# Kernel optimization log

Measured on AMD Instinct MI355X. Metric: run time of the kernel, lower is better.

## Reference

```python
import jax, jax.numpy as jnp
import numpy as np

N = 200000   # active voxels
B = 2        # batch size
G = 128      # spatial grid extent per axis
CIN = 64
COUT = 64
KS = 3       # kernel size -> 27 offsets
DIL = 1
EPS = 1e-5


def setup_inputs() -> dict:
    rng = np.random.default_rng(0)
    # unique active voxel coordinates over a B x G^3 grid
    lin = rng.choice(B * G * G * G, size=N, replace=False)
    b = lin // (G * G * G)
    r = lin % (G * G * G)
    x = r // (G * G)
    r2 = r % (G * G)
    y = r2 // G
    z = r2 % G
    coords = jnp.asarray(np.stack([b, x, y, z], axis=1).astype(np.int32))
    key = jax.random.key(0)
    ks = jax.random.split(key, 7)
    feats = jax.random.normal(ks[0], (N, CIN), jnp.float32)
    s1 = 1.0 / np.sqrt(KS ** 3 * CIN)
    s2 = 1.0 / np.sqrt(KS ** 3 * COUT)
    return {
        "feats": feats,
        "w1": jax.random.normal(ks[1], (KS ** 3, CIN, COUT), jnp.float32) * s1,
        "g1": 1.0 + 0.1 * jax.random.normal(ks[2], (COUT,), jnp.float32),
        "b1": 0.1 * jax.random.normal(ks[3], (COUT,), jnp.float32),
        "w2": jax.random.normal(ks[4], (KS ** 3, COUT, COUT), jnp.float32) * s2,
        "g2": 1.0 + 0.1 * jax.random.normal(ks[5], (COUT,), jnp.float32),
        "b2": 0.1 * jax.random.normal(ks[6], (COUT,), jnp.float32),
        "coords": coords,
    }


def build_neighbors(coords):
    """Hash (dense) lookup: for each of 27 kernel offsets, the input index of
    the neighboring active voxel (submanifold: output sites == input sites).
    Returns idx [27, N] int32 (0 where invalid) and mask [27, N] bool."""
    n = coords.shape[0]
    lin = ((coords[:, 0] * G + coords[:, 1]) * G + coords[:, 2]) * G + coords[:, 3]
    table = jnp.full((B * G * G * G,), -1, jnp.int32).at[lin].set(
        jnp.arange(n, dtype=jnp.int32))
    offs = jnp.asarray(
        [[dx, dy, dz] for dx in (-1, 0, 1) for dy in (-1, 0, 1) for dz in (-1, 0, 1)],
        dtype=jnp.int32) * DIL                       # [27, 3]
    nxyz = coords[None, :, 1:] + offs[:, None, :]    # [27, N, 3]
    inb = jnp.all((nxyz >= 0) & (nxyz < G), axis=-1)  # [27, N]
    c = jnp.clip(nxyz, 0, G - 1)
    nlin = ((coords[None, :, 0] * G + c[..., 0]) * G + c[..., 1]) * G + c[..., 2]
    idx = table[nlin]                                # [27, N]
    mask = inb & (idx >= 0)
    return jnp.where(mask, idx, 0), mask


def subm_conv(feats, nbr_idx, nbr_mask, w):
    # gather-GEMM-scatter, accumulated per kernel offset
    out = jnp.zeros((feats.shape[0], w.shape[-1]), feats.dtype)
    for k in range(w.shape[0]):
        g = jnp.where(nbr_mask[k][:, None], feats[nbr_idx[k]], 0.0)  # [N, Cin]
        out = out + g @ w[k]
    return out


def sparse_bn(x, gamma, beta):
    m = jnp.mean(x, axis=0)
    v = jnp.var(x, axis=0)
    return (x - m) * jax.lax.rsqrt(v + EPS) * gamma + beta


def reference(feats, w1, g1, b1, w2, g2, b2, coords):
    nbr_idx, nbr_mask = build_neighbors(coords)
    h = jax.nn.relu(sparse_bn(subm_conv(feats, nbr_idx, nbr_mask, w1), g1, b1))
    h = sparse_bn(subm_conv(h, nbr_idx, nbr_mask, w2), g2, b2)
    # shortcut is Identity (in_channels == out_channels, stride == 1)
    return jax.nn.relu(h + feats)
```

## Files before the change

kernel.cpp:

```cpp
#include <hip/hip_runtime.h>


constexpr int N_VOX = 200000;
constexpr int GEXT  = 128;
constexpr int C     = 64;
constexpr int K27   = 27;
constexpr int TBL_N = 2 * GEXT * GEXT * GEXT;
constexpr float EPSF = 1e-5f;

constexpr int NTILE = N_VOX / 16;
constexpr int NBLK  = 512;
constexpr int WHALF = K27 * 2 * 2 * 4 * 16 * 8;

using short8  = __attribute__((ext_vector_type(8))) short;
using floatx4 = __attribute__((ext_vector_type(4))) float;

static __device__ __forceinline__ ushort f2bf(float f) {
  union { float f; unsigned u; } a; a.f = f;
  unsigned r = a.u + 0x7fff + ((a.u >> 16) & 1);
  return (ushort)(r >> 16);
}
static __device__ __forceinline__ float bf2f(ushort h) {
  union { unsigned u; float f; } a; a.u = ((unsigned)h) << 16;
  return a.f;
}

__global__ __launch_bounds__(256) void k_fill_table(int* __restrict__ t,
                                                    ushort* __restrict__ zrow) {
  int i = blockIdx.x * 256 + threadIdx.x;
  if (i < TBL_N) t[i] = -1;
  if (i < 64) zrow[i] = 0;
}

__global__ __launch_bounds__(256) void k_scatter(const int* __restrict__ coords,
                                                 int* __restrict__ t) {
  int n = blockIdx.x * 256 + threadIdx.x;
  if (n >= N_VOX) return;
  int4 c = reinterpret_cast<const int4*>(coords)[n];
  int lin = ((c.x * GEXT + c.y) * GEXT + c.z) * GEXT + c.w;
  t[lin] = n;
}

__global__ __launch_bounds__(256) void k_nbr(const int* __restrict__ coords,
                                             const int* __restrict__ t,
                                             int* __restrict__ nbr) {
  int n = blockIdx.x * 256 + threadIdx.x;
  if (n >= N_VOX) return;
  int4 c = reinterpret_cast<const int4*>(coords)[n];
  int k = 0;
  #pragma unroll
  for (int dx = -1; dx <= 1; ++dx)
    #pragma unroll
    for (int dy = -1; dy <= 1; ++dy)
      #pragma unroll
      for (int dz = -1; dz <= 1; ++dz) {
        int x = c.y + dx, y = c.z + dy, z = c.w + dz;
        int idx = -1;
        if (((unsigned)x < (unsigned)GEXT) & ((unsigned)y < (unsigned)GEXT) &
            ((unsigned)z < (unsigned)GEXT)) {
          int lin = ((c.x * GEXT + x) * GEXT + y) * GEXT + z;
          idx = t[lin];
        }
        nbr[k * N_VOX + n] = idx;
        ++k;
      }
}

__global__ __launch_bounds__(256) void k_cast4(const float* __restrict__ in,
                                               ushort* __restrict__ out, int n4) {
  int i = blockIdx.x * 256 + threadIdx.x;
  if (i >= n4) return;
  float4 v = reinterpret_cast<const float4*>(in)[i];
  ushort4 o;
  o.x = f2bf(v.x); o.y = f2bf(v.y); o.z = f2bf(v.z); o.w = f2bf(v.w);
  reinterpret_cast<ushort4*>(out)[i] = o;
}

__global__ __launch_bounds__(256) void k_castw_p(const float* __restrict__ w,
                                                 ushort* __restrict__ wtp) {
  int i = blockIdx.x * 256 + threadIdx.x;
  if (i >= K27 * 4096) return;
  int k = i >> 12, r = i & 4095, ci = r >> 6, co = r & 63;
  int half = co >> 5, q = (co >> 4) & 1, row = co & 15;
  int ks = ci >> 5, cig = (ci >> 3) & 3, e = ci & 7;
  int dst = ((((half * K27 + k) * 2 + q) * 2 + ks) * 4 + cig) * 128 + row * 8 + e;
  wtp[dst] = f2bf(w[i]);
}

template <bool OUT_BF16>
__global__ __launch_bounds__(512, 1) void k_conv_sp(
    const ushort* __restrict__ fin,
    const ushort* __restrict__ wtp,
    const int* __restrict__ nbr,
    const ushort* __restrict__ zrow,
    void* __restrict__ fout,
    float* __restrict__ part) {
  __shared__ ushort Wl[WHALF];
  __shared__ float sred[8][4][16];

  const int tid  = threadIdx.x;
  const int lane = tid & 63;
  const int wv   = tid >> 6;
  const int half = blockIdx.x & 1;
  const int chunk = blockIdx.x >> 1;
  const int lo = lane & 15, hi = lane >> 4;

  {
    const uint4* src = (const uint4*)(wtp + (size_t)half * WHALF);
    uint4* dst = (uint4*)Wl;
    for (int i = tid; i < WHALF / 8; i += 512) dst[i] = src[i];
  }
  __syncthreads();

  const char* wbase = (const char*)Wl + lane * 16;
  float s8[8], ss8[8];
  #pragma unroll
  for (int j = 0; j < 8; ++j) { s8[j] = 0.f; ss8[j] = 0.f; }

  for (int t = chunk * 8 + wv; t < NTILE; t += 2048) {
    const int n0 = t * 16;
    floatx4 acc0 = {0.f, 0.f, 0.f, 0.f};
    floatx4 acc1 = {0.f, 0.f, 0.f, 0.f};

    int idxs[27];
    #pragma unroll
    for (int k = 0; k < K27; ++k) idxs[k] = nbr[k * N_VOX + n0 + lo];

    #pragma unroll
    for (int k = 0; k < K27; ++k) {
      int idx = idxs[k];
      if (__ballot(idx >= 0)) {
        const char* base = (idx >= 0)
            ? (const char*)fin + ((size_t)idx << 7)
            : (const char*)zrow;
        short8 b0 = *(const short8*)(base + hi * 16);
        short8 b1 = *(const short8*)(base + 64 + hi * 16);
        const char* wb = wbase + k * 4096;
        short8 a00 = *(const short8*)(wb);
        short8 a01 = *(const short8*)(wb + 1024);
        short8 a10 = *(const short8*)(wb + 2048);
        short8 a11 = *(const short8*)(wb + 3072);
        acc0 = __builtin_amdgcn_mfma_f32_16x16x32_bf16(a00, b0, acc0, 0, 0, 0);
        acc0 = __builtin_amdgcn_mfma_f32_16x16x32_bf16(a01, b1, acc0, 0, 0, 0);
        acc1 = __builtin_amdgcn_mfma_f32_16x16x32_bf16(a10, b0, acc1, 0, 0, 0);
        acc1 = __builtin_amdgcn_mfma_f32_16x16x32_bf16(a11, b1, acc1, 0, 0, 0);
      }
    }

    const int vox = n0 + lo;
    const int cb  = half * 32 + hi * 4;
    if (OUT_BF16) {
      ushort* o = (ushort*)fout + ((size_t)vox << 6) + cb;
      ushort4 v0, v1;
      v0.x = f2bf(acc0[0]); v0.y = f2bf(acc0[1]);
      v0.z = f2bf(acc0[2]); v0.w = f2bf(acc0[3]);
      v1.x = f2bf(acc1[0]); v1.y = f2bf(acc1[1]);
      v1.z = f2bf(acc1[2]); v1.w = f2bf(acc1[3]);
      *(ushort4*)o = v0;
      *(ushort4*)(o + 16) = v1;
    } else {
      float* o = (float*)fout + ((size_t)vox << 6) + cb;
      float4 v0 = {acc0[0], acc0[1], acc0[2], acc0[3]};
      float4 v1 = {acc1[0], acc1[1], acc1[2], acc1[3]};
      *(float4*)o = v0;
      *(float4*)(o + 16) = v1;
    }
    #pragma unroll
    for (int r = 0; r < 4; ++r) {
      s8[r]     += acc0[r];  ss8[r]     += acc0[r] * acc0[r];
      s8[4 + r] += acc1[r];  ss8[4 + r] += acc1[r] * acc1[r];
    }
  }

  #pragma unroll
  for (int j = 0; j < 8; ++j) {
    float s = s8[j], ss = ss8[j];
    #pragma unroll
    for (int m = 1; m < 16; m <<= 1) {
      s  += __shfl_xor(s, m);
      ss += __shfl_xor(ss, m);
    }
    if (lo == 0) { sred[wv][hi][j] = s; sred[wv][hi][8 + j] = ss; }
  }
  __syncthreads();
  if (tid < 64) {
    int h2 = tid >> 4, j = tid & 15;
    float v = 0.f;
    #pragma unroll
    for (int w = 0; w < 8; ++w) v += sred[w][h2][j];
    int j2 = j & 7;
    int c_local = ((j2 >> 2) << 4) + h2 * 4 + (j2 & 3);
    part[(size_t)blockIdx.x * 64 + (j < 8 ? c_local : 32 + c_local)] = v;
  }
}

__global__ __launch_bounds__(256) void k_bnfin(const float* __restrict__ part,
                                               const float* __restrict__ gamma,
                                               const float* __restrict__ beta,
                                               float* __restrict__ ab) {
  __shared__ float red[256][2];
  int tid = threadIdx.x;
  int c = tid & 63, g = tid >> 6;
  int half = c >> 5, lc = c & 31;
  float s = 0.f, ss = 0.f;
  for (int ch = g; ch < NBLK / 2; ch += 4) {
    const float* p = part + (size_t)(ch * 2 + half) * 64;
    s += p[lc]; ss += p[32 + lc];
  }
  red[tid][0] = s; red[tid][1] = ss;
  __syncthreads();
  if (tid < 64) {
    s  = red[tid][0] + red[tid + 64][0] + red[tid + 128][0] + red[tid + 192][0];
    ss = red[tid][1] + red[tid + 64][1] + red[tid + 128][1] + red[tid + 192][1];
    float mean = s / (float)N_VOX;
    float var  = ss / (float)N_VOX - mean * mean;
    float a = gamma[tid] * rsqrtf(var + EPSF);
    ab[tid]      = a;
    ab[64 + tid] = beta[tid] - mean * a;
  }
}

__global__ __launch_bounds__(256) void k_bnrelu_bf(ushort* __restrict__ x,
                                                   const float* __restrict__ ab) {
  int i = blockIdx.x * 256 + threadIdx.x;
  ushort4 v = reinterpret_cast<ushort4*>(x)[i];
  int cb = (i * 4) & 63;
  v.x = f2bf(fmaxf(bf2f(v.x) * ab[cb]     + ab[64 + cb],     0.f));
  v.y = f2bf(fmaxf(bf2f(v.y) * ab[cb + 1] + ab[64 + cb + 1], 0.f));
  v.z = f2bf(fmaxf(bf2f(v.z) * ab[cb + 2] + ab[64 + cb + 2], 0.f));
  v.w = f2bf(fmaxf(bf2f(v.w) * ab[cb + 3] + ab[64 + cb + 3], 0.f));
  reinterpret_cast<ushort4*>(x)[i] = v;
}

__global__ __launch_bounds__(256) void k_final4(float* __restrict__ h2,
                                                const ushort* __restrict__ fb,
                                                const float* __restrict__ ab) {
  int i = blockIdx.x * 256 + threadIdx.x;
  float4 a = reinterpret_cast<float4*>(h2)[i];
  ushort4 f = reinterpret_cast<const ushort4*>(fb)[i];
  int cb = (i * 4) & 63;
  float4 o;
  o.x = fmaxf(a.x * ab[cb]     + ab[64 + cb]     + bf2f(f.x), 0.f);
  o.y = fmaxf(a.y * ab[cb + 1] + ab[64 + cb + 1] + bf2f(f.y), 0.f);
  o.z = fmaxf(a.z * ab[cb + 2] + ab[64 + cb + 2] + bf2f(f.z), 0.f);
  o.w = fmaxf(a.w * ab[cb + 3] + ab[64 + cb + 3] + bf2f(f.w), 0.f);
  reinterpret_cast<float4*>(h2)[i] = o;
}

extern "C" void kernel_launch(void* const* d_in, const int* in_sizes, int n_in,
                              void* d_out, int out_size, void* d_ws, size_t ws_size,
                              hipStream_t stream) {
  const float* feats  = (const float*)d_in[0];
  const float* w1     = (const float*)d_in[1];
  const float* g1     = (const float*)d_in[2];
  const float* b1     = (const float*)d_in[3];
  const float* w2     = (const float*)d_in[4];
  const float* g2     = (const float*)d_in[5];
  const float* b2     = (const float*)d_in[6];
  const int*   coords = (const int*)d_in[7];
  float* out = (float*)d_out;

  char* ws = (char*)d_ws;
  int*    table = (int*)ws;     ws += (size_t)TBL_N * 4;
  int*    nbr   = (int*)ws;     ws += (size_t)K27 * N_VOX * 4;
  ushort* fb    = (ushort*)ws;  ws += (size_t)N_VOX * C * 2;
  ushort* h1    = (ushort*)ws;  ws += (size_t)N_VOX * C * 2;
  ushort* wtp1  = (ushort*)ws;  ws += (size_t)2 * WHALF * 2;
  ushort* wtp2  = (ushort*)ws;  ws += (size_t)2 * WHALF * 2;
  float*  part  = (float*)ws;   ws += (size_t)NBLK * 64 * 4;
  float*  ab1   = (float*)ws;   ws += 512;
  float*  ab2   = (float*)ws;   ws += 512;
  ushort* zrow  = (ushort*)ws;  ws += 128;

  const int NC4 = N_VOX * C / 4;
  const int VBLK = NC4 / 256;

  k_fill_table<<<(TBL_N + 255) / 256, 256, 0, stream>>>(table, zrow);
  k_scatter<<<(N_VOX + 255) / 256, 256, 0, stream>>>(coords, table);
  k_nbr<<<(N_VOX + 255) / 256, 256, 0, stream>>>(coords, table, nbr);

  k_cast4<<<VBLK, 256, 0, stream>>>(feats, fb, NC4);
  k_castw_p<<<(K27 * 4096 + 255) / 256, 256, 0, stream>>>(w1, wtp1);
  k_castw_p<<<(K27 * 4096 + 255) / 256, 256, 0, stream>>>(w2, wtp2);

  k_conv_sp<true><<<NBLK, 512, 0, stream>>>(fb, wtp1, nbr, zrow, h1, part);
  k_bnfin<<<1, 256, 0, stream>>>(part, g1, b1, ab1);
  k_bnrelu_bf<<<VBLK, 256, 0, stream>>>(h1, ab1);

  k_conv_sp<false><<<NBLK, 512, 0, stream>>>(h1, wtp2, nbr, zrow, out, part);
  k_bnfin<<<1, 256, 0, stream>>>(part, g2, b2, ab2);
  k_final4<<<VBLK, 256, 0, stream>>>(out, fb, ab2);
}
```

Measured before the change: 343.5 us.

## Reorder voxels spatially, switch conv to 32x32 MFMA with global weights

Builds a spatially sorted permutation of voxels (count, scan, compact over the hash table) and runs both convolutions in that order, so neighbour gathers hit nearby rows and the cache works better. The conv kernel now uses 32x32x16 bf16 MFMA reading weights straight from global memory instead of staging them in LDS. It launches one block per 128 voxels with an XCD-aware block mapping and higher occupancy, and scatters the final output back through the permutation. The residual now reads fp32 feats directly. This adds several preprocessing kernels and relies on the weight reads being served from cache.

```diff
diff --git a/kernel.cpp b/kernel.cpp
--- a/kernel.cpp
+++ b/kernel.cpp
@@ -7,13 +7,10 @@
 constexpr int K27   = 27;
 constexpr int TBL_N = 2 * GEXT * GEXT * GEXT;
 constexpr float EPSF = 1e-5f;
-
-constexpr int NTILE = N_VOX / 16;
-constexpr int NBLK  = 512;
-constexpr int WHALF = K27 * 2 * 2 * 4 * 16 * 8;
-
-using short8  = __attribute__((ext_vector_type(8))) short;
-using floatx4 = __attribute__((ext_vector_type(4))) float;
+constexpr int NCBLK = 1563;
+
+using short8   = __attribute__((ext_vector_type(8))) short;
+using floatx16 = __attribute__((ext_vector_type(16))) float;
 
 static __device__ __forceinline__ ushort f2bf(float f) {
   union { float f; unsigned u; } a; a.f = f;
@@ -25,10 +22,12 @@
   return a.f;
 }
 
-__global__ __launch_bounds__(256) void k_fill_table(int* __restrict__ t,
-                                                    ushort* __restrict__ zrow) {
+__global__ __launch_bounds__(256) void k_fill(int* __restrict__ t,
+                                              int* __restrict__ bsum,
+                                              ushort* __restrict__ zrow) {
   int i = blockIdx.x * 256 + threadIdx.x;
   if (i < TBL_N) t[i] = -1;
+  if (i < 4096) bsum[i] = 0;
   if (i < 64) zrow[i] = 0;
 }
 
@@ -41,12 +40,66 @@
   t[lin] = n;
 }
 
-__global__ __launch_bounds__(256) void k_nbr(const int* __restrict__ coords,
-                                             const int* __restrict__ t,
-                                             int* __restrict__ nbr) {
+__global__ __launch_bounds__(256) void k_count(const int* __restrict__ coords,
+                                               int* __restrict__ bsum) {
   int n = blockIdx.x * 256 + threadIdx.x;
   if (n >= N_VOX) return;
   int4 c = reinterpret_cast<const int4*>(coords)[n];
+  int lin = ((c.x * GEXT + c.y) * GEXT + c.z) * GEXT + c.w;
+  atomicAdd(&bsum[lin >> 10], 1);
+}
+
+__global__ __launch_bounds__(1024) void k_scan(const int* __restrict__ bsum,
+                                               int* __restrict__ boff) {
+  __shared__ int sc[1024];
+  int t = threadIdx.x;
+  int v0 = bsum[t * 4], v1 = bsum[t * 4 + 1], v2 = bsum[t * 4 + 2],
+      v3 = bsum[t * 4 + 3];
+  int s = v0 + v1 + v2 + v3;
+  sc[t] = s;
+  __syncthreads();
+  for (int off = 1; off < 1024; off <<= 1) {
+    int x = (t >= off) ? sc[t - off] : 0;
+    __syncthreads();
+    sc[t] += x;
+    __syncthreads();
+  }
+  int excl = sc[t] - s;
+  boff[t * 4]     = excl;
+  boff[t * 4 + 1] = excl + v0;
+  boff[t * 4 + 2] = excl + v0 + v1;
+  boff[t * 4 + 3] = excl + v0 + v1 + v2;
+}
+
+__global__ __launch_bounds__(1024) void k_compact(int* __restrict__ table,
+                                                  const int* __restrict__ boff,
+                                                  int* __restrict__ perm) {
+  __shared__ int wsum[16];
+  int i = blockIdx.x * 1024 + threadIdx.x;
+  int orig = table[i];
+  bool valid = orig >= 0;
+  unsigned long long bal = __ballot(valid);
+  int lane = threadIdx.x & 63, wv = threadIdx.x >> 6;
+  int before = __popcll(bal & ((1ull << lane) - 1ull));
+  if (lane == 0) wsum[wv] = __popcll(bal);
+  __syncthreads();
+  int woff = 0;
+  for (int w = 0; w < 16; ++w) woff += (w < wv) ? wsum[w] : 0;
+  if (valid) {
+    int j = boff[blockIdx.x] + woff + before;
+    perm[j] = orig;
+    table[i] = j;
+  }
+}
+
+__global__ __launch_bounds__(256) void k_nbrp(const int* __restrict__ coords,
+                                              const int* __restrict__ table,
+                                              const int* __restrict__ perm,
+                                              int* __restrict__ nbrp) {
+  int j = blockIdx.x * 256 + threadIdx.x;
+  if (j >= N_VOX) return;
+  int orig = perm[j];
+  int4 c = reinterpret_cast<const int4*>(coords)[orig];
   int k = 0;
   #pragma unroll
   for (int dx = -1; dx <= 1; ++dx)
@@ -55,142 +108,129 @@
       #pragma unroll
       for (int dz = -1; dz <= 1; ++dz) {
         int x = c.y + dx, y = c.z + dy, z = c.w + dz;
-        int idx = -1;
+        int rank = -1;
         if (((unsigned)x < (unsigned)GEXT) & ((unsigned)y < (unsigned)GEXT) &
             ((unsigned)z < (unsigned)GEXT)) {
           int lin = ((c.x * GEXT + x) * GEXT + y) * GEXT + z;
-          idx = t[lin];
+          rank = table[lin];
         }
-        nbr[k * N_VOX + n] = idx;
+        nbrp[k * N_VOX + j] = rank;
         ++k;
       }
 }
 
-__global__ __launch_bounds__(256) void k_cast4(const float* __restrict__ in,
-                                               ushort* __restrict__ out, int n4) {
-  int i = blockIdx.x * 256 + threadIdx.x;
-  if (i >= n4) return;
-  float4 v = reinterpret_cast<const float4*>(in)[i];
+__global__ __launch_bounds__(256) void k_gcast(const float* __restrict__ feats,
+                                               const int* __restrict__ perm,
+                                               ushort* __restrict__ fbp) {
+  int i = blockIdx.x * 256 + threadIdx.x;
+  int j = i >> 4, seg = i & 15;
+  int p = perm[j];
+  float4 v = reinterpret_cast<const float4*>(feats)[(p << 4) + seg];
   ushort4 o;
   o.x = f2bf(v.x); o.y = f2bf(v.y); o.z = f2bf(v.z); o.w = f2bf(v.w);
-  reinterpret_cast<ushort4*>(out)[i] = o;
-}
-
-__global__ __launch_bounds__(256) void k_castw_p(const float* __restrict__ w,
-                                                 ushort* __restrict__ wtp) {
+  reinterpret_cast<ushort4*>(fbp)[i] = o;
+}
+
+__global__ __launch_bounds__(256) void k_castw(const float* __restrict__ w,
+                                               ushort* __restrict__ wp) {
   int i = blockIdx.x * 256 + threadIdx.x;
   if (i >= K27 * 4096) return;
   int k = i >> 12, r = i & 4095, ci = r >> 6, co = r & 63;
-  int half = co >> 5, q = (co >> 4) & 1, row = co & 15;
-  int ks = ci >> 5, cig = (ci >> 3) & 3, e = ci & 7;
-  int dst = ((((half * K27 + k) * 2 + q) * 2 + ks) * 4 + cig) * 128 + row * 8 + e;
-  wtp[dst] = f2bf(w[i]);
+  int ch = co >> 5, row = co & 31;
+  int ks = ci >> 4, hi1 = (ci >> 3) & 1, e = ci & 7;
+  int dst = ((((k * 2 + ch) * 4 + ks) * 2 + hi1) << 8) + row * 8 + e;
+  wp[dst] = f2bf(w[i]);
 }
 
 template <bool OUT_BF16>
-__global__ __launch_bounds__(512, 1) void k_conv_sp(
+__global__ __launch_bounds__(512, 4) void k_conv32(
     const ushort* __restrict__ fin,
-    const ushort* __restrict__ wtp,
-    const int* __restrict__ nbr,
+    const ushort* __restrict__ wp,
+    const int* __restrict__ nbrp,
+    const int* __restrict__ perm,
     const ushort* __restrict__ zrow,
     void* __restrict__ fout,
     float* __restrict__ part) {
-  __shared__ ushort Wl[WHALF];
-  __shared__ float sred[8][4][16];
-
-  const int tid  = threadIdx.x;
-  const int lane = tid & 63;
-  const int wv   = tid >> 6;
-  const int half = blockIdx.x & 1;
-  const int chunk = blockIdx.x >> 1;
-  const int lo = lane & 15, hi = lane >> 4;
-
-  {
-    const uint4* src = (const uint4*)(wtp + (size_t)half * WHALF);
-    uint4* dst = (uint4*)Wl;
-    for (int i = tid; i < WHALF / 8; i += 512) dst[i] = src[i];
-  }
-  __syncthreads();
-
-  const char* wbase = (const char*)Wl + lane * 16;
-  float s8[8], ss8[8];
+  __shared__ float sred[8][2][32];
+  const int tid = threadIdx.x, lane = tid & 63, wv = tid >> 6;
+  const int lo = lane & 31, hi = lane >> 5;
+  const int ch = wv & 1, vh = wv >> 1;
+  const int xcd = blockIdx.x & 7, bi = blockIdx.x >> 3;
+  const int tb = xcd * 195 + (xcd < 3 ? xcd : 3) + bi;
+  const int n0 = tb * 128 + vh * 32;
+
+  float s16[16], ss16[16];
   #pragma unroll
-  for (int j = 0; j < 8; ++j) { s8[j] = 0.f; ss8[j] = 0.f; }
-
-  for (int t = chunk * 8 + wv; t < NTILE; t += 2048) {
-    const int n0 = t * 16;
-    floatx4 acc0 = {0.f, 0.f, 0.f, 0.f};
-    floatx4 acc1 = {0.f, 0.f, 0.f, 0.f};
-
-    int idxs[27];
-    #pragma unroll
-    for (int k = 0; k < K27; ++k) idxs[k] = nbr[k * N_VOX + n0 + lo];
-
+  for (int j = 0; j < 16; ++j) { s16[j] = 0.f; ss16[j] = 0.f; }
+
+  if (n0 < N_VOX) {
+    floatx16 acc;
+    #pragma unroll
+    for (int j = 0; j < 16; ++j) acc[j] = 0.f;
+
+    const char* wbase = (const char*)wp + (ch << 12) + (lane << 4);
     #pragma unroll
     for (int k = 0; k < K27; ++k) {
-      int idx = idxs[k];
+      int idx = nbrp[k * N_VOX + n0 + lo];
       if (__ballot(idx >= 0)) {
         const char* base = (idx >= 0)
             ? (const char*)fin + ((size_t)idx << 7)
             : (const char*)zrow;
-        short8 b0 = *(const short8*)(base + hi * 16);
-        short8 b1 = *(const short8*)(base + 64 + hi * 16);
-        const char* wb = wbase + k * 4096;
-        short8 a00 = *(const short8*)(wb);
-        short8 a01 = *(const short8*)(wb + 1024);
-        short8 a10 = *(const short8*)(wb + 2048);
-        short8 a11 = *(const short8*)(wb + 3072);
-        acc0 = __builtin_amdgcn_mfma_f32_16x16x32_bf16(a00, b0, acc0, 0, 0, 0);
-        acc0 = __builtin_amdgcn_mfma_f32_16x16x32_bf16(a01, b1, acc0, 0, 0, 0);
-        acc1 = __builtin_amdgcn_mfma_f32_16x16x32_bf16(a10, b0, acc1, 0, 0, 0);
-        acc1 = __builtin_amdgcn_mfma_f32_16x16x32_bf16(a11, b1, acc1, 0, 0, 0);
+        const char* wk = wbase + (k << 13);
+        #pragma unroll
+        for (int ks = 0; ks < 4; ++ks) {
+          short8 bf = *(const short8*)(base + (ks << 5) + (hi << 4));
+          short8 af = *(const short8*)(wk + (ks << 10));
+          acc = __builtin_amdgcn_mfma_f32_32x32x16_bf16(af, bf, acc, 0, 0, 0);
+        }
       }
     }
 
-    const int vox = n0 + lo;
-    const int cb  = half * 32 + hi * 4;
     if (OUT_BF16) {
-      ushort* o = (ushort*)fout + ((size_t)vox << 6) + cb;
-      ushort4 v0, v1;
-      v0.x = f2bf(acc0[0]); v0.y = f2bf(acc0[1]);
-      v0.z = f2bf(acc0[2]); v0.w = f2bf(acc0[3]);
-      v1.x = f2bf(acc1[0]); v1.y = f2bf(acc1[1]);
-      v1.z = f2bf(acc1[2]); v1.w = f2bf(acc1[3]);
-      *(ushort4*)o = v0;
-      *(ushort4*)(o + 16) = v1;
+      ushort* o = (ushort*)fout + ((size_t)(n0 + lo) << 6) + (ch << 5) + (hi << 2);
+      #pragma unroll
+      for (int rg = 0; rg < 4; ++rg) {
+        ushort4 v;
+        v.x = f2bf(acc[rg * 4 + 0]); v.y = f2bf(acc[rg * 4 + 1]);
+        v.z = f2bf(acc[rg * 4 + 2]); v.w = f2bf(acc[rg * 4 + 3]);
+        *(ushort4*)(o + (rg << 3)) = v;
+      }
     } else {
-      float* o = (float*)fout + ((size_t)vox << 6) + cb;
-      float4 v0 = {acc0[0], acc0[1], acc0[2], acc0[3]};
-      float4 v1 = {acc1[0], acc1[1], acc1[2], acc1[3]};
-      *(float4*)o = v0;
-      *(float4*)(o + 16) = v1;
+      int p = perm[n0 + lo];
+      float* o = (float*)fout + ((size_t)p << 6) + (ch << 5) + (hi << 2);
+      #pragma unroll
+      for (int rg = 0; rg < 4; ++rg) {
+        float4 v = {acc[rg * 4 + 0], acc[rg * 4 + 1],
+                    acc[rg * 4 + 2], acc[rg * 4 + 3]};
+        *(float4*)(o + (rg << 3)) = v;
+      }
     }
     #pragma unroll
-    for (int r = 0; r < 4; ++r) {
-      s8[r]     += acc0[r];  ss8[r]     += acc0[r] * acc0[r];
-      s8[4 + r] += acc1[r];  ss8[4 + r] += acc1[r] * acc1[r];
+    for (int j = 0; j < 16; ++j) {
+      float v = acc[j];
+      s16[j] += v; ss16[j] += v * v;
     }
   }
 
   #pragma unroll
-  for (int j = 0; j < 8; ++j) {
-    float s = s8[j], ss = ss8[j];
-    #pragma unroll
-    for (int m = 1; m < 16; m <<= 1) {
-      s  += __shfl_xor(s, m);
-      ss += __shfl_xor(ss, m);
+  for (int j = 0; j < 16; ++j) {
+    float s = s16[j], ss = ss16[j];
+    #pragma unroll
+    for (int m = 1; m < 32; m <<= 1) {
+      s += __shfl_xor(s, m); ss += __shfl_xor(ss, m);
     }
-    if (lo == 0) { sred[wv][hi][j] = s; sred[wv][hi][8 + j] = ss; }
-  }
-  __syncthreads();
-  if (tid < 64) {
-    int h2 = tid >> 4, j = tid & 15;
+    if (lo == 0) { sred[wv][hi][j] = s; sred[wv][hi][16 + j] = ss; }
+  }
+  __syncthreads();
+  if (tid < 128) {
+    int halfsel = tid >> 6, c = tid & 63;
+    int chh = c >> 5, w32 = c & 31;
+    int rg = w32 >> 3, hi1 = (w32 >> 2) & 1, r3 = c & 3;
+    int j = halfsel * 16 + rg * 4 + r3;
     float v = 0.f;
     #pragma unroll
-    for (int w = 0; w < 8; ++w) v += sred[w][h2][j];
-    int j2 = j & 7;
-    int c_local = ((j2 >> 2) << 4) + h2 * 4 + (j2 & 3);
-    part[(size_t)blockIdx.x * 64 + (j < 8 ? c_local : 32 + c_local)] = v;
+    for (int vhh = 0; vhh < 4; ++vhh) v += sred[vhh * 2 + chh][hi1][j];
+    part[(size_t)blockIdx.x * 128 + tid] = v;
   }
 }
 
@@ -198,21 +238,19 @@
                                                const float* __restrict__ gamma,
                                                const float* __restrict__ beta,
                                                float* __restrict__ ab) {
-  __shared__ float red[256][2];
+  __shared__ float red[256];
+  __shared__ float fin[128];
   int tid = threadIdx.x;
-  int c = tid & 63, g = tid >> 6;
-  int half = c >> 5, lc = c & 31;
-  float s = 0.f, ss = 0.f;
-  for (int ch = g; ch < NBLK / 2; ch += 4) {
-    const float* p = part + (size_t)(ch * 2 + half) * 64;
-    s += p[lc]; ss += p[32 + lc];
-  }
-  red[tid][0] = s; red[tid][1] = ss;
+  int e = tid & 127, g = tid >> 7;
+  float s = 0.f;
+  for (int b = g; b < NCBLK; b += 2) s += part[(size_t)b * 128 + e];
+  red[tid] = s;
+  __syncthreads();
+  if (tid < 128) fin[tid] = red[tid] + red[tid + 128];
   __syncthreads();
   if (tid < 64) {
-    s  = red[tid][0] + red[tid + 64][0] + red[tid + 128][0] + red[tid + 192][0];
-    ss = red[tid][1] + red[tid + 64][1] + red[tid + 128][1] + red[tid + 192][1];
-    float mean = s / (float)N_VOX;
+    float su = fin[tid], ss = fin[64 + tid];
+    float mean = su / (float)N_VOX;
     float var  = ss / (float)N_VOX - mean * mean;
     float a = gamma[tid] * rsqrtf(var + EPSF);
     ab[tid]      = a;
@@ -220,30 +258,36 @@
   }
 }
 
-__global__ __launch_bounds__(256) void k_bnrelu_bf(ushort* __restrict__ x,
-                                                   const float* __restrict__ ab) {
-  int i = blockIdx.x * 256 + threadIdx.x;
-  ushort4 v = reinterpret_cast<ushort4*>(x)[i];
-  int cb = (i * 4) & 63;
-  v.x = f2bf(fmaxf(bf2f(v.x) * ab[cb]     + ab[64 + cb],     0.f));
-  v.y = f2bf(fmaxf(bf2f(v.y) * ab[cb + 1] + ab[64 + cb + 1], 0.f));
-  v.z = f2bf(fmaxf(bf2f(v.z) * ab[cb + 2] + ab[64 + cb + 2], 0.f));
-  v.w = f2bf(fmaxf(bf2f(v.w) * ab[cb + 3] + ab[64 + cb + 3], 0.f));
-  reinterpret_cast<ushort4*>(x)[i] = v;
+__global__ __launch_bounds__(256) void k_bnrelu8(ushort* __restrict__ x,
+                                                 const float* __restrict__ ab) {
+  int i = blockIdx.x * 256 + threadIdx.x;
+  ushort4 v0 = reinterpret_cast<ushort4*>(x)[i * 2];
+  ushort4 v1 = reinterpret_cast<ushort4*>(x)[i * 2 + 1];
+  int cb = (i * 8) & 63;
+  v0.x = f2bf(fmaxf(bf2f(v0.x) * ab[cb]     + ab[64 + cb],     0.f));
+  v0.y = f2bf(fmaxf(bf2f(v0.y) * ab[cb + 1] + ab[64 + cb + 1], 0.f));
+  v0.z = f2bf(fmaxf(bf2f(v0.z) * ab[cb + 2] + ab[64 + cb + 2], 0.f));
+  v0.w = f2bf(fmaxf(bf2f(v0.w) * ab[cb + 3] + ab[64 + cb + 3], 0.f));
+  v1.x = f2bf(fmaxf(bf2f(v1.x) * ab[cb + 4] + ab[64 + cb + 4], 0.f));
+  v1.y = f2bf(fmaxf(bf2f(v1.y) * ab[cb + 5] + ab[64 + cb + 5], 0.f));
+  v1.z = f2bf(fmaxf(bf2f(v1.z) * ab[cb + 6] + ab[64 + cb + 6], 0.f));
+  v1.w = f2bf(fmaxf(bf2f(v1.w) * ab[cb + 7] + ab[64 + cb + 7], 0.f));
+  reinterpret_cast<ushort4*>(x)[i * 2]     = v0;
+  reinterpret_cast<ushort4*>(x)[i * 2 + 1] = v1;
 }
 
 __global__ __launch_bounds__(256) void k_final4(float* __restrict__ h2,
-                                                const ushort* __restrict__ fb,
+                                                const float* __restrict__ feats,
                                                 const float* __restrict__ ab) {
   int i = blockIdx.x * 256 + threadIdx.x;
   float4 a = reinterpret_cast<float4*>(h2)[i];
-  ushort4 f = reinterpret_cast<const ushort4*>(fb)[i];
+  float4 f = reinterpret_cast<const float4*>(feats)[i];
   int cb = (i * 4) & 63;
   float4 o;
-  o.x = fmaxf(a.x * ab[cb]     + ab[64 + cb]     + bf2f(f.x), 0.f);
-  o.y = fmaxf(a.y * ab[cb + 1] + ab[64 + cb + 1] + bf2f(f.y), 0.f);
-  o.z = fmaxf(a.z * ab[cb + 2] + ab[64 + cb + 2] + bf2f(f.z), 0.f);
-  o.w = fmaxf(a.w * ab[cb + 3] + ab[64 + cb + 3] + bf2f(f.w), 0.f);
+  o.x = fmaxf(a.x * ab[cb]     + ab[64 + cb]     + f.x, 0.f);
+  o.y = fmaxf(a.y * ab[cb + 1] + ab[64 + cb + 1] + f.y, 0.f);
+  o.z = fmaxf(a.z * ab[cb + 2] + ab[64 + cb + 2] + f.z, 0.f);
+  o.w = fmaxf(a.w * ab[cb + 3] + ab[64 + cb + 3] + f.w, 0.f);
   reinterpret_cast<float4*>(h2)[i] = o;
 }
 
@@ -262,32 +306,34 @@
 
   char* ws = (char*)d_ws;
   int*    table = (int*)ws;     ws += (size_t)TBL_N * 4;
-  int*    nbr   = (int*)ws;     ws += (size_t)K27 * N_VOX * 4;
-  ushort* fb    = (ushort*)ws;  ws += (size_t)N_VOX * C * 2;
-  ushort* h1    = (ushort*)ws;  ws += (size_t)N_VOX * C * 2;
-  ushort* wtp1  = (ushort*)ws;  ws += (size_t)2 * WHALF * 2;
-  ushort* wtp2  = (ushort*)ws;  ws += (size_t)2 * WHALF * 2;
-  float*  part  = (float*)ws;   ws += (size_t)NBLK * 64 * 4;
+  int*    nbrp  = (int*)ws;     ws += (size_t)K27 * N_VOX * 4;
+  ushort* fbp   = (ushort*)ws;  ws += (size_t)N_VOX * C * 2;
+  ushort* h1p   = (ushort*)ws;  ws += (size_t)N_VOX * C * 2;
+  int*    perm  = (int*)ws;     ws += (size_t)N_VOX * 4;
+  ushort* wp1   = (ushort*)ws;  ws += (size_t)K27 * 4096 * 2;
+  ushort* wp2   = (ushort*)ws;  ws += (size_t)K27 * 4096 * 2;
+  int*    bsum  = (int*)ws;     ws += 4096 * 4;
+  int*    boff  = (int*)ws;     ws += 4096 * 4;
   float*  ab1   = (float*)ws;   ws += 512;
   float*  ab2   = (float*)ws;   ws += 512;
   ushort* zrow  = (ushort*)ws;  ws += 128;
-
-  const int NC4 = N_VOX * C / 4;
-  const int VBLK = NC4 / 256;
-
-  k_fill_table<<<(TBL_N + 255) / 256, 256, 0, stream>>>(table, zrow);
+  float*  part  = (float*)table;
+
+  k_fill<<<TBL_N / 256, 256, 0, stream>>>(table, bsum, zrow);
   k_scatter<<<(N_VOX + 255) / 256, 256, 0, stream>>>(coords, table);
-  k_nbr<<<(N_VOX + 255) / 256, 256, 0, stream>>>(coords, table, nbr);
-
-  k_cast4<<<VBLK, 256, 0, stream>>>(feats, fb, NC4);
-  k_castw_p<<<(K27 * 4096 + 255) / 256, 256, 0, stream>>>(w1, wtp1);
-  k_castw_p<<<(K27 * 4096 + 255) / 256, 256, 0, stream>>>(w2, wtp2);
-
-  k_conv_sp<true><<<NBLK, 512, 0, stream>>>(fb, wtp1, nbr, zrow, h1, part);
+  k_count<<<(N_VOX + 255) / 256, 256, 0, stream>>>(coords, bsum);
+  k_scan<<<1, 1024, 0, stream>>>(bsum, boff);
+  k_compact<<<TBL_N / 1024, 1024, 0, stream>>>(table, boff, perm);
+  k_nbrp<<<(N_VOX + 255) / 256, 256, 0, stream>>>(coords, table, perm, nbrp);
+  k_gcast<<<N_VOX * 16 / 256, 256, 0, stream>>>(feats, perm, fbp);
+  k_castw<<<(K27 * 4096 + 255) / 256, 256, 0, stream>>>(w1, wp1);
+  k_castw<<<(K27 * 4096 + 255) / 256, 256, 0, stream>>>(w2, wp2);
+
+  k_conv32<true><<<NCBLK, 512, 0, stream>>>(fbp, wp1, nbrp, perm, zrow, h1p, part);
   k_bnfin<<<1, 256, 0, stream>>>(part, g1, b1, ab1);
-  k_bnrelu_bf<<<VBLK, 256, 0, stream>>>(h1, ab1);
-
-  k_conv_sp<false><<<NBLK, 512, 0, stream>>>(h1, wtp2, nbr, zrow, out, part);
+  k_bnrelu8<<<N_VOX * 8 / 256, 256, 0, stream>>>(h1p, ab1);
+
+  k_conv32<false><<<NCBLK, 512, 0, stream>>>(h1p, wp2, nbrp, perm, zrow, out, part);
   k_bnfin<<<1, 256, 0, stream>>>(part, g2, b2, ab2);
-  k_final4<<<VBLK, 256, 0, stream>>>(out, fb, ab2);
-}
+  k_final4<<<N_VOX * 64 / 4 / 256, 256, 0, stream>>>(out, feats, ab2);
+}
```

Measured after the change: 685.8 us. 99.7% more time.
